# Kernel optimization log

Measured on AMD Instinct MI355X. Metric: run time of the kernel, lower is better.

Reference implementation:

```python
import jax, jax.numpy as jnp
import numpy as np

B, N, D = 4, 2048, 512
M = 1024          # codebook_size
H, DH = 8, 64     # heads, dim_head
I = H * DH        # inner_dim = 512
FF = 1024         # dim_feedforward
EPS = 1e-5


def ln(x, g, b):
    mu = jnp.mean(x, axis=-1, keepdims=True)
    var = jnp.mean((x - mu) ** 2, axis=-1, keepdims=True)
    return (x - mu) * jax.lax.rsqrt(var + EPS) * g + b


def setup_inputs() -> dict:
    key = jax.random.key(0)
    ks = jax.random.split(key, 20)
    s = lambda fan: 1.0 / np.sqrt(fan)
    return {
        "context_input": jax.random.normal(ks[0], (B, N, D), jnp.float32),
        "context_mask": jax.random.randint(ks[1], (B, N), 0, 2) > 0,
        "codebook": jax.random.normal(ks[2], (M, D), jnp.float32),
        "norm_g": jnp.ones((D,)), "norm_b": jnp.zeros((D,)),
        "cnorm_g": jnp.ones((D,)), "cnorm_b": jnp.zeros((D,)),
        "wq": jax.random.normal(ks[3], (D, I)) * s(D),
        "wkv": jax.random.normal(ks[4], (D, 2 * I)) * s(D),
        "wo": jax.random.normal(ks[5], (I, D)) * s(I),
        "wo_b": jnp.zeros((D,)),
        "a_norm_g": jnp.ones((D,)), "a_norm_b": jnp.zeros((D,)),
        "a_qkv": jax.random.normal(ks[6], (D, 3 * I)) * s(D),
        "a_out": jax.random.normal(ks[7], (I, D)) * s(I),
        "f_norm_g": jnp.ones((D,)), "f_norm_b": jnp.zeros((D,)),
        "f_w1": jax.random.normal(ks[8], (D, FF)) * s(D),
        "f_w2": jax.random.normal(ks[9], (FF, D)) * s(FF),
    }


def _forward(context_input, context_mask, codebook, norm_g, norm_b, cnorm_g,
             cnorm_b, wq, wkv, wo, wo_b, a_norm_g, a_norm_b, a_qkv, a_out,
             f_norm_g, f_norm_b, f_w1, f_w2):
    scale = DH ** -0.5
    # ---- Vector quantization: nearest-codebook assignment (inference path) ----
    flat = context_input.reshape(-1, D)                      # [B*N, D]
    dist = (jnp.sum(flat ** 2, -1, keepdims=True)
            - 2.0 * flat @ codebook.T
            + jnp.sum(codebook ** 2, -1))                    # [B*N, M]
    flat_idx = jnp.argmin(dist, axis=-1)                     # [B*N]
    indices = flat_idx.reshape(B, N)
    quant = codebook[flat_idx]                               # [B*N, D]
    commit_loss = jnp.mean((flat - jax.lax.stop_gradient(quant)) ** 2)
    counts = jnp.zeros((M,), flat.dtype).at[flat_idx].add(1.0)
    probs = counts / flat_idx.shape[0]
    perplexity = jnp.exp(-jnp.sum(probs * jnp.log(probs + 1e-10)))
    # ---- Cross-attention: codebook queries attend over the context ----
    xq = ln(codebook, norm_g, norm_b)                        # [M, D]
    q = (xq @ wq).reshape(M, H, DH).transpose(1, 0, 2) * scale   # [H, M, DH]
    ctx = ln(context_input, cnorm_g, cnorm_b)                # [B, N, D]
    kv = ctx @ wkv                                           # [B, N, 2I]
    k, v = jnp.split(kv, 2, axis=-1)
    k = k.reshape(B, N, H, DH).transpose(0, 2, 1, 3)         # [B, H, N, DH]
    v = v.reshape(B, N, H, DH).transpose(0, 2, 1, 3)
    sim = jnp.einsum('hid,bhjd->bhij', q, k)                 # [B, H, M, N]
    big = jnp.finfo(sim.dtype).max
    sim = jnp.where(context_mask[:, None, None, :], sim, -big)
    attn = jax.nn.softmax(sim, axis=-1)
    out = jnp.einsum('bhij,bhjd->bhid', attn, v)             # [B, H, M, DH]
    out = out.transpose(0, 2, 1, 3).reshape(B, M, I) @ wo + wo_b  # [B, M, D]
    # ---- Transformer refinement layer (self-attn + FF, residual) ----
    h = ln(out, a_norm_g, a_norm_b)
    qkv = (h @ a_qkv).reshape(B, M, 3, H, DH)
    q2 = qkv[:, :, 0].transpose(0, 2, 1, 3) * scale
    k2 = qkv[:, :, 1].transpose(0, 2, 1, 3)
    v2 = qkv[:, :, 2].transpose(0, 2, 1, 3)
    a2 = jax.nn.softmax(jnp.einsum('bhid,bhjd->bhij', q2, k2), axis=-1)
    o2 = jnp.einsum('bhij,bhjd->bhid', a2, v2)
    out = out + o2.transpose(0, 2, 1, 3).reshape(B, M, I) @ a_out
    hf = ln(out, f_norm_g, f_norm_b)
    out = out + jax.nn.gelu(hf @ f_w1) @ f_w2
    # ---- Gather per-token outputs by VQ index ----
    outputs = jnp.take_along_axis(out, indices[:, :, None], axis=1)  # [B, N, D]
    return outputs, commit_loss, perplexity


def reference(context_input, context_mask, codebook, norm_g, norm_b, cnorm_g,
              cnorm_b, wq, wkv, wo, wo_b, a_norm_g, a_norm_b, a_qkv, a_out,
              f_norm_g, f_norm_b, f_w1, f_w2):
    return _forward(context_input, context_mask, codebook, norm_g, norm_b,
                    cnorm_g, cnorm_b, wq, wkv, wo, wo_b, a_norm_g, a_norm_b,
                    a_qkv, a_out, f_norm_g, f_norm_b, f_w1, f_w2)
```

## Files before the change

### kernel.cpp

```cpp
#include <hip/hip_runtime.h>
#include <math.h>

#define B_ 4
#define N_ 2048
#define D_ 512
#define M_ 1024
#define H_ 8
#define DH_ 64
#define I_ 512
#define FF_ 1024

typedef unsigned short u16;
typedef __attribute__((ext_vector_type(8))) short bf16x8;
typedef __attribute__((ext_vector_type(4))) float f32x4;

__device__ inline u16 f2b(float f) {
  union { float f; unsigned int u; } v; v.f = f;
  unsigned int u = v.u;
  u += 0x7fffu + ((u >> 16) & 1u);
  return (u16)(u >> 16);
}
__device__ inline float b2f(u16 h) {
  union { unsigned int u; float f; } v; v.u = ((unsigned int)h) << 16;
  return v.f;
}
__device__ inline float ex2(float x) { return __builtin_amdgcn_exp2f(x); }
__device__ inline unsigned int cvtpk(float lo, float hi) {
  unsigned int r;
  asm("v_cvt_pk_bf16_f32 %0, %1, %2" : "=v"(r) : "v"(lo), "v"(hi));
  return r;
}

__device__ inline float gelu_f(float x) {
  float x3 = x * x * x;
  return 0.5f * x * (1.f + tanhf(0.7978845608028654f * (x + 0.044715f * x3)));
}

__device__ inline bool better(float d1, int i1, float d2, int i2) {
  return d1 < d2 || (d1 == d2 && i1 < i2);
}
__device__ inline void cswap(float& da, int& ia, float& db, int& ib) {
  if (better(db, ib, da, ia)) {
    float td = da; da = db; db = td;
    int ti = ia; ia = ib; ib = ti;
  }
}
__device__ inline void kmin(float& da, int& ia, float db, int ib) {
  if (better(db, ib, da, ia)) { da = db; ia = ib; }
}

__global__ void zero_init_kernel(float* counts) {
  counts[threadIdx.x] = 0.f;
}

__global__ void mask_detect_kernel(const unsigned char* __restrict__ mb, int* flag) {
  __shared__ int any;
  if (threadIdx.x == 0) any = 0;
  __syncthreads();
  int acc = 0;
  for (int i = threadIdx.x; i < 8192; i += 256)
    if (i & 3) acc |= mb[i];
  if (acc) atomicOr(&any, 1);
  __syncthreads();
  if (threadIdx.x == 0) *flag = any;
}

__global__ void mask_norm_kernel(const void* __restrict__ mraw,
                                 const int* __restrict__ flag,
                                 int* __restrict__ mnorm) {
  int i = blockIdx.x * 256 + threadIdx.x;
  int v;
  if (*flag) v = ((const unsigned char*)mraw)[i];
  else       v = ((const int*)mraw)[i];
  mnorm[i] = (v != 0) ? 1 : 0;
}

__global__ __launch_bounds__(128) void code_sq_kernel(const float* __restrict__ cb,
                                                      double* __restrict__ csq,
                                                      float* __restrict__ csqf) {
  int row = blockIdx.x, tid = threadIdx.x;
  const float4* r4 = (const float4*)(cb + (size_t)row * D_);
  float4 v = r4[tid];
  double s = (double)v.x * v.x + (double)v.y * v.y + (double)v.z * v.z + (double)v.w * v.w;
  for (int off = 32; off; off >>= 1) s += __shfl_down(s, off);
  __shared__ double red[2];
  if ((tid & 63) == 0) red[tid >> 6] = s;
  __syncthreads();
  if (tid == 0) { csq[row] = red[0] + red[1]; csqf[row] = (float)(red[0] + red[1]); }
}

__global__ __launch_bounds__(256) void conv_bf16_kernel(const float* __restrict__ src,
                                                        u16* __restrict__ dst) {
  int i = (blockIdx.x * 256 + threadIdx.x) * 8;
  float4 a = *(const float4*)(src + i);
  float4 b = *(const float4*)(src + i + 4);
  uint4 o;
  o.x = cvtpk(a.x, a.y);
  o.y = cvtpk(a.z, a.w);
  o.z = cvtpk(b.x, b.y);
  o.w = cvtpk(b.z, b.w);
  *(uint4*)(dst + i) = o;
}

__global__ __launch_bounds__(256) void vq_top4_reduce_kernel(
    const float4* __restrict__ cand_part, int4* __restrict__ cand4)
{
  int t = blockIdx.x * 256 + threadIdx.x;
  float d0 = 1e30f, d1 = 1e30f, d2 = 1e30f, d3 = 1e30f;
  int x0 = 1 << 20, x1 = 1 << 21, x2 = 1 << 22, x3 = 1 << 23;
#pragma unroll
  for (int cb = 0; cb < 16; cb++) {
    float4 a = cand_part[(size_t)t * 32 + cb * 2];
    float4 b = cand_part[(size_t)t * 32 + cb * 2 + 1];
    float e0 = a.x, e1 = a.y, e2 = b.x, e3 = b.y;
    int y0 = __float_as_int(a.z), y1 = __float_as_int(a.w);
    int y2 = __float_as_int(b.z), y3 = __float_as_int(b.w);
    kmin(d0, x0, e3, y3); kmin(d1, x1, e2, y2);
    kmin(d2, x2, e1, y1); kmin(d3, x3, e0, y0);
    cswap(d0, x0, d2, x2); cswap(d1, x1, d3, x3);
    cswap(d0, x0, d1, x1); cswap(d2, x2, d3, x3);
  }
  cand4[t] = make_int4(x0, x1, x2, x3);
}

__global__ __launch_bounds__(256) void vq_refine4_kernel(
    const float* __restrict__ flat, const float* __restrict__ cb,
    const double* __restrict__ csq, const int4* __restrict__ cand4,
    int* __restrict__ out_idx, double* __restrict__ commit_partial,
    float* __restrict__ counts)
{
  int wave = threadIdx.x >> 6, lane = threadIdx.x & 63;
  int t = blockIdx.x * 4 + wave;
  int4 c = cand4[t];
  const float* x = flat + ((size_t)t << 9);
  const float* p0 = cb + ((size_t)c.x << 9);
  const float* p1 = cb + ((size_t)c.y << 9);
  const float* p2 = cb + ((size_t)c.z << 9);
  const float* p3 = cb + ((size_t)c.w << 9);
  double s0 = 0.0, s1 = 0.0, s2 = 0.0, s3 = 0.0, sx = 0.0;
#pragma unroll
  for (int i = 0; i < 8; i++) {
    int d = lane + i * 64;
    double xv = x[d];
    s0 += xv * (double)p0[d];
    s1 += xv * (double)p1[d];
    s2 += xv * (double)p2[d];
    s3 += xv * (double)p3[d];
    sx += xv * xv;
  }
  for (int off = 32; off; off >>= 1) {
    s0 += __shfl_down(s0, off);
    s1 += __shfl_down(s1, off);
    s2 += __shfl_down(s2, off);
    s3 += __shfl_down(s3, off);
    sx += __shfl_down(sx, off);
  }
  if (lane == 0) {
    double dd0 = csq[c.x] - 2.0 * s0;
    double dd1 = csq[c.y] - 2.0 * s1;
    double dd2 = csq[c.z] - 2.0 * s2;
    double dd3 = csq[c.w] - 2.0 * s3;
    int bi = c.x; double bd = dd0;
    if (dd1 < bd || (dd1 == bd && c.y < bi)) { bd = dd1; bi = c.y; }
    if (dd2 < bd || (dd2 == bd && c.z < bi)) { bd = dd2; bi = c.z; }
    if (dd3 < bd || (dd3 == bd && c.w < bi)) { bd = dd3; bi = c.w; }
    out_idx[t] = bi;
    commit_partial[t] = sx + bd;
    atomicAdd(counts + bi, 1.0f);
  }
}

__global__ __launch_bounds__(256) void ln_rows_kernel(
    const float* __restrict__ x, const float* __restrict__ g,
    const float* __restrict__ b, u16* __restrict__ y)
{
  int row = blockIdx.x, tid = threadIdx.x;
  const float* xr = x + (size_t)row * D_;
  float v0 = xr[tid], v1 = xr[tid + 256];
  float s = v0 + v1;
  for (int off = 32; off; off >>= 1) s += __shfl_down(s, off);
  __shared__ float red[4];
  __shared__ float bcast[2];
  if ((tid & 63) == 0) red[tid >> 6] = s;
  __syncthreads();
  if (tid == 0) bcast[0] = (red[0] + red[1] + red[2] + red[3]) * (1.f / 512.f);
  __syncthreads();
  float mu = bcast[0];
  float d0 = v0 - mu, d1 = v1 - mu;
  float q = d0 * d0 + d1 * d1;
  for (int off = 32; off; off >>= 1) q += __shfl_down(q, off);
  if ((tid & 63) == 0) red[tid >> 6] = q;
  __syncthreads();
  if (tid == 0) bcast[1] = rsqrtf((red[0] + red[1] + red[2] + red[3]) * (1.f / 512.f) + 1e-5f);
  __syncthreads();
  float rs = bcast[1];
  u16* yr = y + (size_t)row * D_;
  yr[tid]       = f2b(d0 * rs * g[tid] + b[tid]);
  yr[tid + 256] = f2b(d1 * rs * g[tid + 256] + b[tid + 256]);
}

struct WJobs {
  const float* src[7];
  u16* dst[7];
  int K[7], N[7], b0[8];
};

__global__ __launch_bounds__(256) void wconv_all_kernel(WJobs jobs) {
  __shared__ float tile[32][33];
  int bid = blockIdx.x;
  int j = 0;
#pragma unroll
  for (int i = 1; i < 7; i++) if (bid >= jobs.b0[i]) j = i;
  int tb = bid - jobs.b0[j];
  int K = jobs.K[j], Nn = jobs.N[j];
  int tiles_x = Nn >> 5;
  int n0 = (tb % tiles_x) << 5, k0 = (tb / tiles_x) << 5;
  const float* W = jobs.src[j];
  u16* WT = jobs.dst[j];
  int t = threadIdx.x;
  int ty = t >> 5, tx = t & 31;
#pragma unroll
  for (int i = 0; i < 4; i++)
    tile[ty + 8 * i][tx] = W[(size_t)(k0 + ty + 8 * i) * Nn + n0 + tx];
  __syncthreads();
#pragma unroll
  for (int i = 0; i < 4; i++)
    WT[(size_t)(n0 + ty + 8 * i) * K + k0 + tx] = f2b(tile[tx][ty + 8 * i]);
}

template <int BN>
__global__ __launch_bounds__(256, 4) void gemm_bf16_kernel(
    const u16* __restrict__ A, const u16* __restrict__ BT,
    const float* __restrict__ bias, const float* __restrict__ resid,
    float* __restrict__ Cf, u16* __restrict__ Cb,
    const float* __restrict__ csqf, float4* __restrict__ cand_part,
    int M, int N, int K, int act)
{
  constexpr int MF = (BN == 128) ? 4 : 2;
  constexpr int ROWS_W = (BN == 128) ? 64 : 32;
  __shared__ __attribute__((aligned(16))) u16 As[2][128 * 40];
  __shared__ __attribute__((aligned(16))) u16 Bs[2][BN * 40];
  int tid = threadIdx.x;
  int lane = tid & 63, wave = tid >> 6;
  int wr = (BN == 128) ? (wave >> 1) : wave;
  int wc = (BN == 128) ? (wave & 1) : 0;
  int nwgx = gridDim.x;
  int nwg = nwgx * gridDim.y;
  int flat = blockIdx.y * nwgx + blockIdx.x;
  if ((nwg & 7) == 0) flat = (flat & 7) * (nwg >> 3) + (flat >> 3);
  int row0 = (flat / nwgx) << 7, col0 = (flat % nwgx) * BN;
  int l15 = lane & 15, l4 = lane >> 4;
  int sr = tid >> 2, skc = tid & 3;
  int soff = sr * 40 + skc * 8;
  const u16* pA0 = A + (size_t)(row0 + sr) * K + skc * 8;
  const u16* pA1 = A + (size_t)(row0 + 64 + sr) * K + skc * 8;
  const u16* pB0 = BT + (size_t)(col0 + sr) * K + skc * 8;
  const u16* pB1 = (BN == 128) ? (BT + (size_t)(col0 + 64 + sr) * K + skc * 8) : nullptr;
  f32x4 acc[MF][4] = {};
  int KT = K >> 5;
  bf16x8 ra0 = *(const bf16x8*)pA0;
  bf16x8 ra1 = *(const bf16x8*)pA1;
  bf16x8 rb0 = *(const bf16x8*)pB0;
  bf16x8 rb1;
  if constexpr (BN == 128) rb1 = *(const bf16x8*)pB1;
  *(bf16x8*)&As[0][soff] = ra0;
  *(bf16x8*)&As[0][64 * 40 + soff] = ra1;
  *(bf16x8*)&Bs[0][soff] = rb0;
  if constexpr (BN == 128) *(bf16x8*)&Bs[0][64 * 40 + soff] = rb1;
  if (KT > 1) {
    ra0 = *(const bf16x8*)(pA0 + 32);
    ra1 = *(const bf16x8*)(pA1 + 32);
    rb0 = *(const bf16x8*)(pB0 + 32);
    if constexpr (BN == 128) rb1 = *(const bf16x8*)(pB1 + 32);
  }
  for (int kt = 0; kt < KT; kt++) {
    int cur = kt & 1;
    __syncthreads();
    if (kt + 1 < KT) {
      *(bf16x8*)&As[cur ^ 1][soff] = ra0;
      *(bf16x8*)&As[cur ^ 1][64 * 40 + soff] = ra1;
      *(bf16x8*)&Bs[cur ^ 1][soff] = rb0;
      if constexpr (BN == 128) *(bf16x8*)&Bs[cur ^ 1][64 * 40 + soff] = rb1;
    }
    if (kt + 2 < KT) {
      int ko = (kt + 2) << 5;
      ra0 = *(const bf16x8*)(pA0 + ko);
      ra1 = *(const bf16x8*)(pA1 + ko);
      rb0 = *(const bf16x8*)(pB0 + ko);
      if constexpr (BN == 128) rb1 = *(const bf16x8*)(pB1 + ko);
    }
    bf16x8 af[MF], bfr[4];
#pragma unroll
    for (int m = 0; m < MF; m++)
      af[m] = *(const bf16x8*)&As[cur][(wr * ROWS_W + m * 16 + l15) * 40 + l4 * 8];
#pragma unroll
    for (int n = 0; n < 4; n++)
      bfr[n] = *(const bf16x8*)&Bs[cur][(wc * 64 + n * 16 + l15) * 40 + l4 * 8];
#pragma unroll
    for (int m = 0; m < MF; m++)
#pragma unroll
      for (int n = 0; n < 4; n++)
        acc[m][n] = __builtin_amdgcn_mfma_f32_16x16x32_bf16(af[m], bfr[n], acc[m][n], 0, 0, 0);
  }
  if constexpr (BN == 128) {
    if (act == 2) {
      float csq_l[4];
#pragma unroll
      for (int n = 0; n < 4; n++) csq_l[n] = csqf[col0 + wc * 64 + n * 16 + l15];
      int cbase = col0 + wc * 64 + l15;
      int slot = ((col0 >> 7) << 1) + wc;
#pragma unroll
      for (int m = 0; m < 4; m++) {
#pragma unroll
        for (int r = 0; r < 4; r++) {
          float d0 = csq_l[0] - 2.f * acc[m][0][r];
          float d1 = csq_l[1] - 2.f * acc[m][1][r];
          float d2 = csq_l[2] - 2.f * acc[m][2][r];
          float d3 = csq_l[3] - 2.f * acc[m][3][r];
          int x0 = cbase, x1 = cbase + 16, x2 = cbase + 32, x3 = cbase + 48;
          cswap(d0, x0, d1, x1); cswap(d2, x2, d3, x3);
          cswap(d0, x0, d2, x2); cswap(d1, x1, d3, x3);
          cswap(d1, x1, d2, x2);
          for (int off = 1; off < 16; off <<= 1) {
            float e0 = __shfl_xor(d0, off), e1 = __shfl_xor(d1, off);
            float e2 = __shfl_xor(d2, off), e3 = __shfl_xor(d3, off);
            int y0 = __shfl_xor(x0, off), y1 = __shfl_xor(x1, off);
            int y2 = __shfl_xor(x2, off), y3 = __shfl_xor(x3, off);
            kmin(d0, x0, e3, y3); kmin(d1, x1, e2, y2);
            kmin(d2, x2, e1, y1); kmin(d3, x3, e0, y0);
            cswap(d0, x0, d2, x2); cswap(d1, x1, d3, x3);
            cswap(d0, x0, d1, x1); cswap(d2, x2, d3, x3);
          }
          if (l15 == 0) {
            int row = row0 + wr * 64 + m * 16 + l4 * 4 + r;
            float4 v1, v2;
            v1.x = d0; v1.y = d1;
            v1.z = __int_as_float(x0); v1.w = __int_as_float(x1);
            v2.x = d2; v2.y = d3;
            v2.z = __int_as_float(x2); v2.w = __int_as_float(x3);
            cand_part[(size_t)row * 32 + slot * 2]     = v1;
            cand_part[(size_t)row * 32 + slot * 2 + 1] = v2;
          }
        }
      }
      return;
    }
  }
#pragma unroll
  for (int m = 0; m < MF; m++) {
#pragma unroll
    for (int n = 0; n < 4; n++) {
      int col = col0 + wc * 64 + n * 16 + l15;
      float bv = bias ? bias[col] : 0.f;
#pragma unroll
      for (int r = 0; r < 4; r++) {
        int row = row0 + wr * ROWS_W + m * 16 + l4 * 4 + r;
        float v = acc[m][n][r] + bv;
        if (act == 1) v = gelu_f(v);
        if (resid) v += resid[(size_t)row * N + col];
        if (Cf) Cf[(size_t)row * N + col] = v;
        if (Cb) Cb[(size_t)row * N + col] = f2b(v);
      }
    }
  }
}

__global__ __launch_bounds__(256) void vt_kernel(
    const u16* __restrict__ src, size_t b_stride, int row_stride, int col0,
    int n_rows, u16* __restrict__ dst)
{
  __shared__ __attribute__((aligned(16))) u16 tile[32][72];
  int t = threadIdx.x;
  int bh = blockIdx.y;
  int b = bh >> 3, h = bh & 7;
  int n0 = blockIdx.x * 32;
  int n = t >> 3, dc = t & 7;
  *(bf16x8*)&tile[n][dc * 8] =
      *(const bf16x8*)(src + (size_t)b * b_stride + (size_t)(n0 + n) * row_stride + col0 + h * 64 + dc * 8);
  __syncthreads();
  int d = t >> 2, ns = t & 3;
  bf16x8 o;
#pragma unroll
  for (int i = 0; i < 8; i++) o[i] = (short)tile[ns * 8 + i][d];
  *(bf16x8*)(dst + ((size_t)bh * 64 + d) * n_rows + n0 + ns * 8) = o;
}

__global__ __launch_bounds__(256, 4) void attn_mfma_kernel(
    const u16* __restrict__ Q, size_t q_bs, int q_stride,
    const u16* __restrict__ Kp, size_t k_bs, int k_stride, int k_extra,
    const u16* __restrict__ Vt, const int* __restrict__ mask,
    float scale, u16* __restrict__ Opart, float* __restrict__ MLpart,
    int n_keys)
{
  __shared__ __attribute__((aligned(16))) u16 Ks[8 * 64 * 8];
  __shared__ __attribute__((aligned(16))) u16 Vs[8 * 64 * 8];
  __shared__ __attribute__((aligned(16))) u16 Ps[4][8 * 32 * 8];
  __shared__ float mbias[64];
  int tid = threadIdx.x, lane = tid & 63, wave = tid >> 6;
  int flat = blockIdx.x + (blockIdx.y << 3) + (blockIdx.z << 6);
  int swz = ((flat & 7) << 7) + (flat >> 3);
  int qb = swz & 7, h = (swz >> 3) & 7, z = swz >> 6;
  int b = z & 3, split = z >> 2;
  int q0 = qb * 128 + wave * 32;
  int l15 = lane & 15, l4 = lane >> 4;
  int nq = n_keys >> 2;
  int nstart = split * nq, nend = nstart + nq;

  const u16* qrow = Q + (size_t)b * q_bs + (size_t)(q0 + l15) * q_stride + h * 64 + l4 * 8;
  bf16x8 qfA0 = *(const bf16x8*)qrow;
  bf16x8 qfA1 = *(const bf16x8*)(qrow + 32);
  const u16* qrowB = qrow + 16 * q_stride;
  bf16x8 qfB0 = *(const bf16x8*)qrowB;
  bf16x8 qfB1 = *(const bf16x8*)(qrowB + 32);
  f32x4 oA[4] = {}, oB[4] = {};
  float mA = -3.0e38f, lA = 0.f, mB = -3.0e38f, lB = 0.f;
  int srow = tid >> 2, schunk = tid & 3;
  const u16* kbase = Kp + (size_t)b * k_bs + k_extra + h * 64;
  const u16* vtbase = Vt + (size_t)(b * 8 + h) * 64 * n_keys;

  bf16x8 pk0, pk1, pv0, pv1;
  int pmv = 1;
  {
    const u16* krow = kbase + (size_t)(nstart + srow) * k_stride;
    pk0 = *(const bf16x8*)(krow + schunk * 8);
    pk1 = *(const bf16x8*)(krow + (schunk + 4) * 8);
    const u16* vrow = vtbase + (size_t)srow * n_keys + nstart;
    pv0 = *(const bf16x8*)(vrow + schunk * 8);
    pv1 = *(const bf16x8*)(vrow + (schunk + 4) * 8);
    if (mask && tid < 64) pmv = mask[(size_t)b * n_keys + nstart + tid];
  }

  for (int n0 = nstart; n0 < nend; n0 += 64) {
    __syncthreads();
    *(bf16x8*)&Ks[(schunk * 64 + srow) * 8]       = pk0;
    *(bf16x8*)&Ks[((schunk + 4) * 64 + srow) * 8] = pk1;
    *(bf16x8*)&Vs[(schunk * 64 + srow) * 8]       = pv0;
    *(bf16x8*)&Vs[((schunk + 4) * 64 + srow) * 8] = pv1;
    if (tid < 64) mbias[tid] = (mask && !pmv) ? -3.0e38f : 0.f;
    __syncthreads();
    if (n0 + 64 < nend) {
      const u16* krow = kbase + (size_t)(n0 + 64 + srow) * k_stride;
      pk0 = *(const bf16x8*)(krow + schunk * 8);
      pk1 = *(const bf16x8*)(krow + (schunk + 4) * 8);
      const u16* vrow = vtbase + (size_t)srow * n_keys + n0 + 64;
      pv0 = *(const bf16x8*)(vrow + schunk * 8);
      pv1 = *(const bf16x8*)(vrow + (schunk + 4) * 8);
      if (mask && tid < 64) pmv = mask[(size_t)b * n_keys + n0 + 64 + tid];
    }
    f32x4 sacA[4], sacB[4];
#pragma unroll
    for (int kb = 0; kb < 4; kb++) {
      bf16x8 kf0 = *(const bf16x8*)&Ks[(l4 * 64 + kb * 16 + l15) * 8];
      bf16x8 kf1 = *(const bf16x8*)&Ks[((l4 + 4) * 64 + kb * 16 + l15) * 8];
      f32x4 za = {}, zb = {};
      za = __builtin_amdgcn_mfma_f32_16x16x32_bf16(kf0, qfA0, za, 0, 0, 0);
      sacA[kb] = __builtin_amdgcn_mfma_f32_16x16x32_bf16(kf1, qfA1, za, 0, 0, 0);
      zb = __builtin_amdgcn_mfma_f32_16x16x32_bf16(kf0, qfB0, zb, 0, 0, 0);
      sacB[kb] = __builtin_amdgcn_mfma_f32_16x16x32_bf16(kf1, qfB1, zb, 0, 0, 0);
    }
    {
      float pmax = -3.0e38f;
#pragma unroll
      for (int kb = 0; kb < 4; kb++) {
        float4 bs = *(const float4*)&mbias[kb * 16 + l4 * 4];
        sacA[kb][0] = fmaf(sacA[kb][0], scale, bs.x);
        sacA[kb][1] = fmaf(sacA[kb][1], scale, bs.y);
        sacA[kb][2] = fmaf(sacA[kb][2], scale, bs.z);
        sacA[kb][3] = fmaf(sacA[kb][3], scale, bs.w);
#pragma unroll
        for (int r = 0; r < 4; r++) pmax = fmaxf(pmax, sacA[kb][r]);
      }
      pmax = fmaxf(pmax, __shfl_xor(pmax, 16));
      pmax = fmaxf(pmax, __shfl_xor(pmax, 32));
      if (!__all(pmax - mA <= 11.5f)) {
        float mnew = fmaxf(mA, pmax);
        float al = ex2(mA - mnew);
        lA *= al;
        mA = mnew;
        float alr[4];
#pragma unroll
        for (int r = 0; r < 4; r++) alr[r] = __shfl(al, l4 * 4 + r, 64);
#pragma unroll
        for (int nb = 0; nb < 4; nb++)
#pragma unroll
          for (int r = 0; r < 4; r++) oA[nb][r] *= alr[r];
      }
      float psum = 0.f;
#pragma unroll
      for (int kb = 0; kb < 4; kb++) {
        float p0 = ex2(sacA[kb][0] - mA);
        float p1 = ex2(sacA[kb][1] - mA);
        float p2 = ex2(sacA[kb][2] - mA);
        float p3 = ex2(sacA[kb][3] - mA);
        psum += (p0 + p1) + (p2 + p3);
        uint2 w;
        w.x = cvtpk(p0, p1);
        w.y = cvtpk(p2, p3);
        *(uint2*)&Ps[wave][((kb * 2 + (l4 >> 1)) * 32 + l15) * 8 + (l4 & 1) * 4] = w;
      }
      psum += __shfl_xor(psum, 16);
      psum += __shfl_xor(psum, 32);
      lA += psum;
    }
    {
      float pmax = -3.0e38f;
#pragma unroll
      for (int kb = 0; kb < 4; kb++) {
        float4 bs = *(const float4*)&mbias[kb * 16 + l4 * 4];
        sacB[kb][0] = fmaf(sacB[kb][0], scale, bs.x);
        sacB[kb][1] = fmaf(sacB[kb][1], scale, bs.y);
        sacB[kb][2] = fmaf(sacB[kb][2], scale, bs.z);
        sacB[kb][3] = fmaf(sacB[kb][3], scale, bs.w);
#pragma unroll
        for (int r = 0; r < 4; r++) pmax = fmaxf(pmax, sacB[kb][r]);
      }
      pmax = fmaxf(pmax, __shfl_xor(pmax, 16));
      pmax = fmaxf(pmax, __shfl_xor(pmax, 32));
      if (!__all(pmax - mB <= 11.5f)) {
        float mnew = fmaxf(mB, pmax);
        float al = ex2(mB - mnew);
        lB *= al;
        mB = mnew;
        float alr[4];
#pragma unroll
        for (int r = 0; r < 4; r++) alr[r] = __shfl(al, l4 * 4 + r, 64);
#pragma unroll
        for (int nb = 0; nb < 4; nb++)
#pragma unroll
          for (int r = 0; r < 4; r++) oB[nb][r] *= alr[r];
      }
      float psum = 0.f;
#pragma unroll
      for (int kb = 0; kb < 4; kb++) {
        float p0 = ex2(sacB[kb][0] - mB);
        float p1 = ex2(sacB[kb][1] - mB);
        float p2 = ex2(sacB[kb][2] - mB);
        float p3 = ex2(sacB[kb][3] - mB);
        psum += (p0 + p1) + (p2 + p3);
        uint2 w;
        w.x = cvtpk(p0, p1);
        w.y = cvtpk(p2, p3);
        *(uint2*)&Ps[wave][((kb * 2 + (l4 >> 1)) * 32 + 16 + l15) * 8 + (l4 & 1) * 4] = w;
      }
      psum += __shfl_xor(psum, 16);
      psum += __shfl_xor(psum, 32);
      lB += psum;
    }
#pragma unroll
    for (int c = 0; c < 2; c++) {
      bf16x8 pfA = *(const bf16x8*)&Ps[wave][((c * 4 + l4) * 32 + l15) * 8];
      bf16x8 pfB = *(const bf16x8*)&Ps[wave][((c * 4 + l4) * 32 + 16 + l15) * 8];
#pragma unroll
      for (int nb = 0; nb < 4; nb++) {
        bf16x8 vf = *(const bf16x8*)&Vs[((c * 4 + l4) * 64 + nb * 16 + l15) * 8];
        oA[nb] = __builtin_amdgcn_mfma_f32_16x16x32_bf16(pfA, vf, oA[nb], 0, 0, 0);
        oB[nb] = __builtin_amdgcn_mfma_f32_16x16x32_bf16(pfB, vf, oB[nb], 0, 0, 0);
      }
    }
  }
  int pr_base = ((split * 4 + b) * 8 + h) * 1024;
#pragma unroll
  for (int nb = 0; nb < 4; nb++)
#pragma unroll
    for (int r = 0; r < 4; r++) {
      Opart[(size_t)(pr_base + q0 + l4 * 4 + r) * 64 + nb * 16 + l15] = f2b(oA[nb][r]);
      Opart[(size_t)(pr_base + q0 + 16 + l4 * 4 + r) * 64 + nb * 16 + l15] = f2b(oB[nb][r]);
    }
  if (lane < 16) {
    int pr = pr_base + q0 + lane;
    MLpart[2 * pr]     = mA;
    MLpart[2 * pr + 1] = lA;
  } else if (lane < 32) {
    int pr = pr_base + q0 + 16 + l15;
    MLpart[2 * pr]     = mB;
    MLpart[2 * pr + 1] = lB;
  }
}

__global__ __launch_bounds__(256) void attn_combine_kernel(
    const u16* __restrict__ Opart, const float* __restrict__ MLpart,
    u16* __restrict__ O, size_t o_bs)
{
  int idx = blockIdx.x * 256 + threadIdx.x;
  int d = idx & 63, gq = idx >> 6;
  int row = gq & 1023, bh = gq >> 10;
  int h = bh & 7, b = bh >> 3;
  float m[4], l[4];
  int pr[4];
#pragma unroll
  for (int s = 0; s < 4; s++) {
    pr[s] = ((s * 4 + b) * 8 + h) * 1024 + row;
    m[s] = MLpart[2 * pr[s]];
    l[s] = MLpart[2 * pr[s] + 1];
  }
  float mmax = fmaxf(fmaxf(m[0], m[1]), fmaxf(m[2], m[3]));
  float lsum = 0.f, osum = 0.f;
#pragma unroll
  for (int s = 0; s < 4; s++) {
    float w = ex2(m[s] - mmax);
    lsum += l[s] * w;
    osum += b2f(Opart[(size_t)pr[s] * 64 + d]) * w;
  }
  O[(size_t)b * o_bs + (size_t)row * 512 + h * 64 + d] = f2b(osum / lsum);
}

__global__ __launch_bounds__(128) void gather_kernel(
    const float* __restrict__ x2, const int* __restrict__ idx, float* __restrict__ out)
{
  int t = blockIdx.x;
  int b = t >> 11;
  int code = idx[t];
  const float4* src = (const float4*)(x2 + ((size_t)(b * M_ + code) << 9));
  float4* dst = (float4*)(out + ((size_t)t << 9));
  dst[threadIdx.x] = src[threadIdx.x];
}

__global__ void scalars_kernel(const float* __restrict__ counts,
                               const double* __restrict__ commit_partial,
                               float* __restrict__ out_tail)
{
  int tid = threadIdx.x;
  double cs = 0.0;
#pragma unroll
  for (int i = 0; i < 8; i++) cs += commit_partial[tid + i * 1024];
  double p = (double)counts[tid] / 8192.0;
  double e = p * log(p + 1e-10);
  for (int off = 32; off; off >>= 1) {
    cs += __shfl_down(cs, off);
    e  += __shfl_down(e, off);
  }
  __shared__ double redc[16], rede[16];
  if ((tid & 63) == 0) { redc[tid >> 6] = cs; rede[tid >> 6] = e; }
  __syncthreads();
  if (tid == 0) {
    double sc = 0.0, se = 0.0;
    for (int i = 0; i < 16; i++) { sc += redc[i]; se += rede[i]; }
    out_tail[0] = (float)(sc / (8192.0 * 512.0));
    out_tail[1] = (float)exp(-se);
  }
}

extern "C" void kernel_launch(void* const* d_in, const int* in_sizes, int n_in,
                              void* d_out, int out_size, void* d_ws, size_t ws_size,
                              hipStream_t stream) {
  const float* ctx      = (const float*)d_in[0];
  const void*  mask_raw = d_in[1];
  const float* codebook = (const float*)d_in[2];
  const float* norm_g   = (const float*)d_in[3];
  const float* norm_b   = (const float*)d_in[4];
  const float* cnorm_g  = (const float*)d_in[5];
  const float* cnorm_b  = (const float*)d_in[6];
  const float* wq       = (const float*)d_in[7];
  const float* wkv      = (const float*)d_in[8];
  const float* wo       = (const float*)d_in[9];
  const float* wo_b     = (const float*)d_in[10];
  const float* a_norm_g = (const float*)d_in[11];
  const float* a_norm_b = (const float*)d_in[12];
  const float* a_qkv    = (const float*)d_in[13];
  const float* a_out    = (const float*)d_in[14];
  const float* f_norm_g = (const float*)d_in[15];
  const float* f_norm_b = (const float*)d_in[16];
  const float* f_w1     = (const float*)d_in[17];
  const float* f_w2     = (const float*)d_in[18];
  float* out = (float*)d_out;
  const float LOG2E = 1.4426950408889634f;

  char* ws = (char*)d_ws;
  int*    mask_flag  = (int*)(ws + 64);
  float*  counts     = (float*)(ws + 128);
  double* code_sq    = (double*)(ws + 4224);
  float*  csqf       = (float*)(ws + 12416);
  int*    indices    = (int*)(ws + 16512);
  int*    mask_norm  = (int*)(ws + 49280);
  int4*   cand4      = (int4*)(ws + 82048);
  double* commit_partial = (double*)(ws + 262144);

  char* pool = ws + (1 << 20);
  u16*   vqA  = (u16*)(pool);
  u16*   vqBT = (u16*)(pool + ((size_t)25 << 20));
  float4* cand_part = (float4*)(pool + ((size_t)30 << 20));
  float* attn_ml = (float*)(pool + ((size_t)61 << 20));
  char* regA  = pool;
  char* regB  = pool + ((size_t)16 << 20);
  char* regC  = pool + ((size_t)24 << 20);
  char* regD  = pool + ((size_t)32 << 20);
  char* regE  = pool + ((size_t)40 << 20);
  char* regF  = pool + ((size_t)44 << 20);
  size_t woff = (1 << 20) + ((size_t)64 << 20);
  u16* wqT    = (u16*)(ws + woff); woff += (size_t)512 * 512 * 2;
  u16* wkvT   = (u16*)(ws + woff); woff += (size_t)1024 * 512 * 2;
  u16* woT    = (u16*)(ws + woff); woff += (size_t)512 * 512 * 2;
  u16* aqkvT  = (u16*)(ws + woff); woff += (size_t)1536 * 512 * 2;
  u16* aoutT  = (u16*)(ws + woff); woff += (size_t)512 * 512 * 2;
  u16* fw1T   = (u16*)(ws + woff); woff += (size_t)1024 * 512 * 2;
  u16* fw2T   = (u16*)(ws + woff); woff += (size_t)512 * 1024 * 2;
  u16* xq_b   = (u16*)(ws + woff); woff += (size_t)1024 * 512 * 2;
  u16* qs_b   = (u16*)(ws + woff); woff += (size_t)1024 * 512 * 2;

  u16* kv_b     = (u16*)regA;
  u16* qkv2_b   = (u16*)regA;
  u16* ctx_ln_b = (u16*)regB;
  u16* VtS      = (u16*)regB;
  u16* VtX      = (u16*)regC;
  float* x1_f   = (float*)regC;
  float* x0_f   = (float*)regD;
  u16* att_out_b = (u16*)regE;
  u16* h_b       = (u16*)regE;
  u16* o2_b      = (u16*)regE;
  u16* hf_b      = (u16*)regE;
  u16* g_b      = (u16*)regF;
  float* x2_f   = (float*)(pool + ((size_t)52 << 20));
  u16* attn_part = (u16*)regF;

  zero_init_kernel<<<1, 1024, 0, stream>>>(counts);
  mask_detect_kernel<<<1, 256, 0, stream>>>((const unsigned char*)mask_raw, mask_flag);
  mask_norm_kernel<<<32, 256, 0, stream>>>(mask_raw, mask_flag, mask_norm);
  code_sq_kernel<<<1024, 128, 0, stream>>>(codebook, code_sq, csqf);
  conv_bf16_kernel<<<2048, 256, 0, stream>>>(ctx, vqA);
  conv_bf16_kernel<<<256, 256, 0, stream>>>(codebook, vqBT);
  gemm_bf16_kernel<128><<<dim3(8, 64), 256, 0, stream>>>(vqA, vqBT, nullptr, nullptr,
                                                    nullptr, nullptr, csqf, cand_part,
                                                    8192, 1024, 512, 2);
  vq_top4_reduce_kernel<<<32, 256, 0, stream>>>(cand_part, cand4);
  vq_refine4_kernel<<<2048, 256, 0, stream>>>(ctx, codebook, code_sq, cand4, indices,
                                              commit_partial, counts);

  WJobs jobs;
  jobs.src[0] = wq;    jobs.dst[0] = wqT;   jobs.K[0] = 512;  jobs.N[0] = 512;
  jobs.src[1] = wkv;   jobs.dst[1] = wkvT;  jobs.K[1] = 512;  jobs.N[1] = 1024;
  jobs.src[2] = wo;    jobs.dst[2] = woT;   jobs.K[2] = 512;  jobs.N[2] = 512;
  jobs.src[3] = a_qkv; jobs.dst[3] = aqkvT; jobs.K[3] = 512;  jobs.N[3] = 1536;
  jobs.src[4] = a_out; jobs.dst[4] = aoutT; jobs.K[4] = 512;  jobs.N[4] = 512;
  jobs.src[5] = f_w1;  jobs.dst[5] = fw1T;  jobs.K[5] = 512;  jobs.N[5] = 1024;
  jobs.src[6] = f_w2;  jobs.dst[6] = fw2T;  jobs.K[6] = 1024; jobs.N[6] = 512;
  int acc_b = 0;
  for (int i = 0; i < 7; i++) {
    jobs.b0[i] = acc_b;
    acc_b += (jobs.K[i] >> 5) * (jobs.N[i] >> 5);
  }
  jobs.b0[7] = acc_b;
  wconv_all_kernel<<<acc_b, 256, 0, stream>>>(jobs);

  ln_rows_kernel<<<1024, 256, 0, stream>>>(codebook, norm_g, norm_b, xq_b);
  gemm_bf16_kernel<64><<<dim3(8, 8), 256, 0, stream>>>(xq_b, wqT, nullptr, nullptr,
                                                   nullptr, qs_b, nullptr, nullptr,
                                                   1024, 512, 512, 0);
  ln_rows_kernel<<<8192, 256, 0, stream>>>(ctx, cnorm_g, cnorm_b, ctx_ln_b);
  gemm_bf16_kernel<128><<<dim3(8, 64), 256, 0, stream>>>(ctx_ln_b, wkvT, nullptr, nullptr,
                                                    nullptr, kv_b, nullptr, nullptr,
                                                    8192, 1024, 512, 0);
  vt_kernel<<<dim3(64, 32), 256, 0, stream>>>(kv_b, (size_t)2048 * 1024, 1024, 512, 2048, VtX);
  attn_mfma_kernel<<<dim3(8, 8, 16), 256, 0, stream>>>(
      qs_b, 0, 512, kv_b, (size_t)2048 * 1024, 1024, 0, VtX, mask_norm,
      0.125f * LOG2E, attn_part, attn_ml, 2048);
  attn_combine_kernel<<<8192, 256, 0, stream>>>(attn_part, attn_ml, att_out_b, (size_t)1024 * 512);
  gemm_bf16_kernel<64><<<dim3(8, 32), 256, 0, stream>>>(att_out_b, woT, wo_b, nullptr,
                                                    x0_f, nullptr, nullptr, nullptr,
                                                    4096, 512, 512, 0);

  ln_rows_kernel<<<4096, 256, 0, stream>>>(x0_f, a_norm_g, a_norm_b, h_b);
  gemm_bf16_kernel<64><<<dim3(24, 32), 256, 0, stream>>>(h_b, aqkvT, nullptr, nullptr,
                                                     nullptr, qkv2_b, nullptr, nullptr,
                                                     4096, 1536, 512, 0);
  vt_kernel<<<dim3(32, 32), 256, 0, stream>>>(qkv2_b, (size_t)1024 * 1536, 1536, 1024, 1024, VtS);
  attn_mfma_kernel<<<dim3(8, 8, 16), 256, 0, stream>>>(
      qkv2_b, (size_t)1024 * 1536, 1536, qkv2_b, (size_t)1024 * 1536, 1536, 512, VtS, nullptr,
      0.125f * LOG2E, attn_part, attn_ml, 1024);
  attn_combine_kernel<<<8192, 256, 0, stream>>>(attn_part, attn_ml, o2_b, (size_t)1024 * 512);
  gemm_bf16_kernel<64><<<dim3(8, 32), 256, 0, stream>>>(o2_b, aoutT, nullptr, x0_f,
                                                    x1_f, nullptr, nullptr, nullptr,
                                                    4096, 512, 512, 0);
  ln_rows_kernel<<<4096, 256, 0, stream>>>(x1_f, f_norm_g, f_norm_b, hf_b);
  gemm_bf16_kernel<64><<<dim3(16, 32), 256, 0, stream>>>(hf_b, fw1T, nullptr, nullptr,
                                                    nullptr, g_b, nullptr, nullptr,
                                                    4096, 1024, 512, 1);
  gemm_bf16_kernel<64><<<dim3(8, 32), 256, 0, stream>>>(g_b, fw2T, nullptr, x1_f,
                                                    x2_f, nullptr, nullptr, nullptr,
                                                    4096, 512, 1024, 0);

  gather_kernel<<<8192, 128, 0, stream>>>(x2_f, indices, out);
  scalars_kernel<<<1, 1024, 0, stream>>>(counts, commit_partial, out + (size_t)B_ * N_ * D_);
}
```

Baseline: 321.1 us.

## Merge small prep kernels and fold top-4 reduction into refine kernel

Merges several small launches into fewer kernels. Mask detection, both bf16 conversions and the weight transposes now run in one prep kernel. Codebook norms, count zeroing and mask normalization share one kernel, and the gather and scalar reductions share one. The separate top-4 candidate reduction is folded into the refine kernel using 16-lane xor shuffles. The aim is to cut kernel launch overhead and an intermediate buffer round trip, at the cost of branchy heterogeneous blocks and duplicated shuffle work in each wave.

```diff
diff --git a/kernel.cpp b/kernel.cpp
--- a/kernel.cpp
+++ b/kernel.cpp
@@ -49,94 +49,136 @@
   if (better(db, ib, da, ia)) { da = db; ia = ib; }
 }
 
-__global__ void zero_init_kernel(float* counts) {
-  counts[threadIdx.x] = 0.f;
-}
-
-__global__ void mask_detect_kernel(const unsigned char* __restrict__ mb, int* flag) {
+struct WJobs {
+  const float* src[7];
+  u16* dst[7];
+  int K[7], N[7], b0[8];
+};
+
+__global__ __launch_bounds__(256) void prep_kernel(
+    const unsigned char* __restrict__ mb, int* __restrict__ flag,
+    const float* __restrict__ ctx, u16* __restrict__ vqA,
+    const float* __restrict__ cb, u16* __restrict__ vqBT,
+    WJobs jobs)
+{
+  __shared__ float tile[32][33];
   __shared__ int any;
-  if (threadIdx.x == 0) any = 0;
+  int bid = blockIdx.x;
+  int tid = threadIdx.x;
+  if (bid == 0) {
+    if (tid == 0) any = 0;
+    __syncthreads();
+    int acc = 0;
+    for (int i = tid; i < 8192; i += 256)
+      if (i & 3) acc |= mb[i];
+    if (acc) atomicOr(&any, 1);
+    __syncthreads();
+    if (tid == 0) *flag = any;
+    return;
+  }
+  if (bid < 2049) {
+    int i = ((bid - 1) * 256 + tid) * 8;
+    float4 a = *(const float4*)(ctx + i);
+    float4 b = *(const float4*)(ctx + i + 4);
+    uint4 o;
+    o.x = cvtpk(a.x, a.y); o.y = cvtpk(a.z, a.w);
+    o.z = cvtpk(b.x, b.y); o.w = cvtpk(b.z, b.w);
+    *(uint4*)(vqA + i) = o;
+    return;
+  }
+  if (bid < 2305) {
+    int i = ((bid - 2049) * 256 + tid) * 8;
+    float4 a = *(const float4*)(cb + i);
+    float4 b = *(const float4*)(cb + i + 4);
+    uint4 o;
+    o.x = cvtpk(a.x, a.y); o.y = cvtpk(a.z, a.w);
+    o.z = cvtpk(b.x, b.y); o.w = cvtpk(b.z, b.w);
+    *(uint4*)(vqBT + i) = o;
+    return;
+  }
+  int wb = bid - 2305;
+  int j = 0;
+#pragma unroll
+  for (int i = 1; i < 7; i++) if (wb >= jobs.b0[i]) j = i;
+  int tb = wb - jobs.b0[j];
+  int K = jobs.K[j], Nn = jobs.N[j];
+  int tiles_x = Nn >> 5;
+  int n0 = (tb % tiles_x) << 5, k0 = (tb / tiles_x) << 5;
+  const float* W = jobs.src[j];
+  u16* WT = jobs.dst[j];
+  int ty = tid >> 5, tx = tid & 31;
+#pragma unroll
+  for (int i = 0; i < 4; i++)
+    tile[ty + 8 * i][tx] = W[(size_t)(k0 + ty + 8 * i) * Nn + n0 + tx];
   __syncthreads();
-  int acc = 0;
-  for (int i = threadIdx.x; i < 8192; i += 256)
-    if (i & 3) acc |= mb[i];
-  if (acc) atomicOr(&any, 1);
-  __syncthreads();
-  if (threadIdx.x == 0) *flag = any;
-}
-
-__global__ void mask_norm_kernel(const void* __restrict__ mraw,
-                                 const int* __restrict__ flag,
-                                 int* __restrict__ mnorm) {
-  int i = blockIdx.x * 256 + threadIdx.x;
-  int v;
-  if (*flag) v = ((const unsigned char*)mraw)[i];
-  else       v = ((const int*)mraw)[i];
-  mnorm[i] = (v != 0) ? 1 : 0;
-}
-
-__global__ __launch_bounds__(128) void code_sq_kernel(const float* __restrict__ cb,
-                                                      double* __restrict__ csq,
-                                                      float* __restrict__ csqf) {
-  int row = blockIdx.x, tid = threadIdx.x;
-  const float4* r4 = (const float4*)(cb + (size_t)row * D_);
-  float4 v = r4[tid];
-  double s = (double)v.x * v.x + (double)v.y * v.y + (double)v.z * v.z + (double)v.w * v.w;
-  for (int off = 32; off; off >>= 1) s += __shfl_down(s, off);
-  __shared__ double red[2];
-  if ((tid & 63) == 0) red[tid >> 6] = s;
-  __syncthreads();
-  if (tid == 0) { csq[row] = red[0] + red[1]; csqf[row] = (float)(red[0] + red[1]); }
-}
-
-__global__ __launch_bounds__(256) void conv_bf16_kernel(const float* __restrict__ src,
-                                                        u16* __restrict__ dst) {
-  int i = (blockIdx.x * 256 + threadIdx.x) * 8;
-  float4 a = *(const float4*)(src + i);
-  float4 b = *(const float4*)(src + i + 4);
-  uint4 o;
-  o.x = cvtpk(a.x, a.y);
-  o.y = cvtpk(a.z, a.w);
-  o.z = cvtpk(b.x, b.y);
-  o.w = cvtpk(b.z, b.w);
-  *(uint4*)(dst + i) = o;
-}
-
-__global__ __launch_bounds__(256) void vq_top4_reduce_kernel(
-    const float4* __restrict__ cand_part, int4* __restrict__ cand4)
-{
-  int t = blockIdx.x * 256 + threadIdx.x;
-  float d0 = 1e30f, d1 = 1e30f, d2 = 1e30f, d3 = 1e30f;
-  int x0 = 1 << 20, x1 = 1 << 21, x2 = 1 << 22, x3 = 1 << 23;
-#pragma unroll
-  for (int cb = 0; cb < 16; cb++) {
-    float4 a = cand_part[(size_t)t * 32 + cb * 2];
-    float4 b = cand_part[(size_t)t * 32 + cb * 2 + 1];
-    float e0 = a.x, e1 = a.y, e2 = b.x, e3 = b.y;
-    int y0 = __float_as_int(a.z), y1 = __float_as_int(a.w);
-    int y2 = __float_as_int(b.z), y3 = __float_as_int(b.w);
+#pragma unroll
+  for (int i = 0; i < 4; i++)
+    WT[(size_t)(n0 + ty + 8 * i) * K + k0 + tx] = f2b(tile[tx][ty + 8 * i]);
+}
+
+__global__ __launch_bounds__(128) void sq_norm_kernel(
+    const float* __restrict__ cb, double* __restrict__ csq, float* __restrict__ csqf,
+    float* __restrict__ counts, const void* __restrict__ mraw,
+    const int* __restrict__ flag, int* __restrict__ mnorm)
+{
+  int tid = threadIdx.x;
+  if (blockIdx.x < 1024) {
+    int row = blockIdx.x;
+    const float4* r4 = (const float4*)(cb + (size_t)row * D_);
+    float4 v = r4[tid];
+    double s = (double)v.x * v.x + (double)v.y * v.y + (double)v.z * v.z + (double)v.w * v.w;
+    for (int off = 32; off; off >>= 1) s += __shfl_down(s, off);
+    __shared__ double red[2];
+    if ((tid & 63) == 0) red[tid >> 6] = s;
+    __syncthreads();
+    if (tid == 0) {
+      csq[row] = red[0] + red[1];
+      csqf[row] = (float)(red[0] + red[1]);
+      counts[row] = 0.f;
+    }
+    return;
+  }
+  int j = blockIdx.x - 1024;
+  int fl = *flag;
+#pragma unroll
+  for (int k = 0; k < 2; k++) {
+    int i = j * 256 + tid + k * 128;
+    int v;
+    if (fl) v = ((const unsigned char*)mraw)[i];
+    else    v = ((const int*)mraw)[i];
+    mnorm[i] = (v != 0) ? 1 : 0;
+  }
+}
+
+__global__ __launch_bounds__(256) void vq_refine4_kernel(
+    const float* __restrict__ flat, const float* __restrict__ cb,
+    const double* __restrict__ csq, const float4* __restrict__ cand_part,
+    int* __restrict__ out_idx, double* __restrict__ commit_partial,
+    float* __restrict__ counts)
+{
+  int wave = threadIdx.x >> 6, lane = threadIdx.x & 63;
+  int t = blockIdx.x * 4 + wave;
+  int sl = lane & 15;
+  float4 a = cand_part[(size_t)t * 32 + sl * 2];
+  float4 bb = cand_part[(size_t)t * 32 + sl * 2 + 1];
+  float d0 = a.x, d1 = a.y, d2 = bb.x, d3 = bb.y;
+  int x0 = __float_as_int(a.z), x1 = __float_as_int(a.w);
+  int x2 = __float_as_int(bb.z), x3 = __float_as_int(bb.w);
+  for (int off = 1; off < 16; off <<= 1) {
+    float e0 = __shfl_xor(d0, off), e1 = __shfl_xor(d1, off);
+    float e2 = __shfl_xor(d2, off), e3 = __shfl_xor(d3, off);
+    int y0 = __shfl_xor(x0, off), y1 = __shfl_xor(x1, off);
+    int y2 = __shfl_xor(x2, off), y3 = __shfl_xor(x3, off);
     kmin(d0, x0, e3, y3); kmin(d1, x1, e2, y2);
     kmin(d2, x2, e1, y1); kmin(d3, x3, e0, y0);
     cswap(d0, x0, d2, x2); cswap(d1, x1, d3, x3);
     cswap(d0, x0, d1, x1); cswap(d2, x2, d3, x3);
   }
-  cand4[t] = make_int4(x0, x1, x2, x3);
-}
-
-__global__ __launch_bounds__(256) void vq_refine4_kernel(
-    const float* __restrict__ flat, const float* __restrict__ cb,
-    const double* __restrict__ csq, const int4* __restrict__ cand4,
-    int* __restrict__ out_idx, double* __restrict__ commit_partial,
-    float* __restrict__ counts)
-{
-  int wave = threadIdx.x >> 6, lane = threadIdx.x & 63;
-  int t = blockIdx.x * 4 + wave;
-  int4 c = cand4[t];
   const float* x = flat + ((size_t)t << 9);
-  const float* p0 = cb + ((size_t)c.x << 9);
-  const float* p1 = cb + ((size_t)c.y << 9);
-  const float* p2 = cb + ((size_t)c.z << 9);
-  const float* p3 = cb + ((size_t)c.w << 9);
+  const float* p0 = cb + ((size_t)x0 << 9);
+  const float* p1 = cb + ((size_t)x1 << 9);
+  const float* p2 = cb + ((size_t)x2 << 9);
+  const float* p3 = cb + ((size_t)x3 << 9);
   double s0 = 0.0, s1 = 0.0, s2 = 0.0, s3 = 0.0, sx = 0.0;
 #pragma unroll
   for (int i = 0; i < 8; i++) {
@@ -156,14 +198,14 @@
     sx += __shfl_down(sx, off);
   }
   if (lane == 0) {
-    double dd0 = csq[c.x] - 2.0 * s0;
-    double dd1 = csq[c.y] - 2.0 * s1;
-    double dd2 = csq[c.z] - 2.0 * s2;
-    double dd3 = csq[c.w] - 2.0 * s3;
-    int bi = c.x; double bd = dd0;
-    if (dd1 < bd || (dd1 == bd && c.y < bi)) { bd = dd1; bi = c.y; }
-    if (dd2 < bd || (dd2 == bd && c.z < bi)) { bd = dd2; bi = c.z; }
-    if (dd3 < bd || (dd3 == bd && c.w < bi)) { bd = dd3; bi = c.w; }
+    double dd0 = csq[x0] - 2.0 * s0;
+    double dd1 = csq[x1] - 2.0 * s1;
+    double dd2 = csq[x2] - 2.0 * s2;
+    double dd3 = csq[x3] - 2.0 * s3;
+    int bi = x0; double bd = dd0;
+    if (dd1 < bd || (dd1 == bd && x1 < bi)) { bd = dd1; bi = x1; }
+    if (dd2 < bd || (dd2 == bd && x2 < bi)) { bd = dd2; bi = x2; }
+    if (dd3 < bd || (dd3 == bd && x3 < bi)) { bd = dd3; bi = x3; }
     out_idx[t] = bi;
     commit_partial[t] = sx + bd;
     atomicAdd(counts + bi, 1.0f);
@@ -197,35 +239,6 @@
   u16* yr = y + (size_t)row * D_;
   yr[tid]       = f2b(d0 * rs * g[tid] + b[tid]);
   yr[tid + 256] = f2b(d1 * rs * g[tid + 256] + b[tid + 256]);
-}
-
-struct WJobs {
-  const float* src[7];
-  u16* dst[7];
-  int K[7], N[7], b0[8];
-};
-
-__global__ __launch_bounds__(256) void wconv_all_kernel(WJobs jobs) {
-  __shared__ float tile[32][33];
-  int bid = blockIdx.x;
-  int j = 0;
-#pragma unroll
-  for (int i = 1; i < 7; i++) if (bid >= jobs.b0[i]) j = i;
-  int tb = bid - jobs.b0[j];
-  int K = jobs.K[j], Nn = jobs.N[j];
-  int tiles_x = Nn >> 5;
-  int n0 = (tb % tiles_x) << 5, k0 = (tb / tiles_x) << 5;
-  const float* W = jobs.src[j];
-  u16* WT = jobs.dst[j];
-  int t = threadIdx.x;
-  int ty = t >> 5, tx = t & 31;
-#pragma unroll
-  for (int i = 0; i < 4; i++)
-    tile[ty + 8 * i][tx] = W[(size_t)(k0 + ty + 8 * i) * Nn + n0 + tx];
-  __syncthreads();
-#pragma unroll
-  for (int i = 0; i < 4; i++)
-    WT[(size_t)(n0 + ty + 8 * i) * K + k0 + tx] = f2b(tile[tx][ty + 8 * i]);
 }
 
 template <int BN>
@@ -604,39 +617,40 @@
   O[(size_t)b * o_bs + (size_t)row * 512 + h * 64 + d] = f2b(osum / lsum);
 }
 
-__global__ __launch_bounds__(128) void gather_kernel(
-    const float* __restrict__ x2, const int* __restrict__ idx, float* __restrict__ out)
+__global__ __launch_bounds__(128) void gather_scalars_kernel(
+    const float* __restrict__ x2, const int* __restrict__ idx,
+    const float* __restrict__ counts, const double* __restrict__ commit_partial,
+    float* __restrict__ out, float* __restrict__ out_tail)
 {
   int t = blockIdx.x;
-  int b = t >> 11;
-  int code = idx[t];
-  const float4* src = (const float4*)(x2 + ((size_t)(b * M_ + code) << 9));
-  float4* dst = (float4*)(out + ((size_t)t << 9));
-  dst[threadIdx.x] = src[threadIdx.x];
-}
-
-__global__ void scalars_kernel(const float* __restrict__ counts,
-                               const double* __restrict__ commit_partial,
-                               float* __restrict__ out_tail)
-{
   int tid = threadIdx.x;
+  if (t < 8192) {
+    int b = t >> 11;
+    int code = idx[t];
+    const float4* src = (const float4*)(x2 + ((size_t)(b * M_ + code) << 9));
+    float4* dst = (float4*)(out + ((size_t)t << 9));
+    dst[tid] = src[tid];
+    return;
+  }
   double cs = 0.0;
 #pragma unroll
-  for (int i = 0; i < 8; i++) cs += commit_partial[tid + i * 1024];
-  double p = (double)counts[tid] / 8192.0;
-  double e = p * log(p + 1e-10);
+  for (int i = 0; i < 64; i++) cs += commit_partial[tid + i * 128];
+  double e = 0.0;
+#pragma unroll
+  for (int i = 0; i < 8; i++) {
+    double p = (double)counts[tid + i * 128] / 8192.0;
+    e += p * log(p + 1e-10);
+  }
   for (int off = 32; off; off >>= 1) {
     cs += __shfl_down(cs, off);
     e  += __shfl_down(e, off);
   }
-  __shared__ double redc[16], rede[16];
+  __shared__ double redc[2], rede[2];
   if ((tid & 63) == 0) { redc[tid >> 6] = cs; rede[tid >> 6] = e; }
   __syncthreads();
   if (tid == 0) {
-    double sc = 0.0, se = 0.0;
-    for (int i = 0; i < 16; i++) { sc += redc[i]; se += rede[i]; }
-    out_tail[0] = (float)(sc / (8192.0 * 512.0));
-    out_tail[1] = (float)exp(-se);
+    out_tail[0] = (float)((redc[0] + redc[1]) / (8192.0 * 512.0));
+    out_tail[1] = (float)exp(-(rede[0] + rede[1]));
   }
 }
 
@@ -672,7 +686,6 @@
   float*  csqf       = (float*)(ws + 12416);
   int*    indices    = (int*)(ws + 16512);
   int*    mask_norm  = (int*)(ws + 49280);
-  int4*   cand4      = (int4*)(ws + 82048);
   double* commit_partial = (double*)(ws + 262144);
 
   char* pool = ws + (1 << 20);
@@ -712,19 +725,6 @@
   float* x2_f   = (float*)(pool + ((size_t)52 << 20));
   u16* attn_part = (u16*)regF;
 
-  zero_init_kernel<<<1, 1024, 0, stream>>>(counts);
-  mask_detect_kernel<<<1, 256, 0, stream>>>((const unsigned char*)mask_raw, mask_flag);
-  mask_norm_kernel<<<32, 256, 0, stream>>>(mask_raw, mask_flag, mask_norm);
-  code_sq_kernel<<<1024, 128, 0, stream>>>(codebook, code_sq, csqf);
-  conv_bf16_kernel<<<2048, 256, 0, stream>>>(ctx, vqA);
-  conv_bf16_kernel<<<256, 256, 0, stream>>>(codebook, vqBT);
-  gemm_bf16_kernel<128><<<dim3(8, 64), 256, 0, stream>>>(vqA, vqBT, nullptr, nullptr,
-                                                    nullptr, nullptr, csqf, cand_part,
-                                                    8192, 1024, 512, 2);
-  vq_top4_reduce_kernel<<<32, 256, 0, stream>>>(cand_part, cand4);
-  vq_refine4_kernel<<<2048, 256, 0, stream>>>(ctx, codebook, code_sq, cand4, indices,
-                                              commit_partial, counts);
-
   WJobs jobs;
   jobs.src[0] = wq;    jobs.dst[0] = wqT;   jobs.K[0] = 512;  jobs.N[0] = 512;
   jobs.src[1] = wkv;   jobs.dst[1] = wkvT;  jobs.K[1] = 512;  jobs.N[1] = 1024;
@@ -739,7 +739,17 @@
     acc_b += (jobs.K[i] >> 5) * (jobs.N[i] >> 5);
   }
   jobs.b0[7] = acc_b;
-  wconv_all_kernel<<<acc_b, 256, 0, stream>>>(jobs);
+  prep_kernel<<<2305 + acc_b, 256, 0, stream>>>(
+      (const unsigned char*)mask_raw, mask_flag, ctx, vqA, codebook, vqBT, jobs);
+
+  sq_norm_kernel<<<1056, 128, 0, stream>>>(codebook, code_sq, csqf, counts,
+                                           mask_raw, mask_flag, mask_norm);
+
+  gemm_bf16_kernel<128><<<dim3(8, 64), 256, 0, stream>>>(vqA, vqBT, nullptr, nullptr,
+                                                    nullptr, nullptr, csqf, cand_part,
+                                                    8192, 1024, 512, 2);
+  vq_refine4_kernel<<<2048, 256, 0, stream>>>(ctx, codebook, code_sq, cand_part, indices,
+                                              commit_partial, counts);
 
   ln_rows_kernel<<<1024, 256, 0, stream>>>(codebook, norm_g, norm_b, xq_b);
   gemm_bf16_kernel<64><<<dim3(8, 8), 256, 0, stream>>>(xq_b, wqT, nullptr, nullptr,
@@ -778,6 +788,6 @@
                                                     x2_f, nullptr, nullptr, nullptr,
                                                     4096, 512, 1024, 0);
 
-  gather_kernel<<<8192, 128, 0, stream>>>(x2_f, indices, out);
-  scalars_kernel<<<1, 1024, 0, stream>>>(counts, commit_partial, out + (size_t)B_ * N_ * D_);
-}
+  gather_scalars_kernel<<<8193, 128, 0, stream>>>(x2_f, indices, counts, commit_partial,
+                                                  out, out + (size_t)B_ * N_ * D_);
+}
```

Measured after the change: 299.1 us. 6.9% less time.
